# Kernel optimization log

Measured on AMD Instinct MI355X. Metric: run time of the kernel, lower is better.

Reference implementation:

```python
import jax, jax.numpy as jnp
import numpy as np

D_MODEL = 768
NUM_HEADS = 12
HEAD_DIM = D_MODEL // NUM_HEADS
B, S = 2, 2048


def setup_inputs() -> dict:
    key = jax.random.key(0)
    ks = jax.random.split(key, 12)
    s = 1.0 / np.sqrt(D_MODEL)
    inp = {
        "query": jax.random.normal(ks[0], (B, S, D_MODEL), jnp.float32),
        "key": jax.random.normal(ks[1], (B, S, D_MODEL), jnp.float32),
        "value": jax.random.normal(ks[2], (B, S, D_MODEL), jnp.float32),
        # causal mask; masked_fill(scores, mask == 0, -inf)
        "mask": jnp.tril(jnp.ones((S, S), jnp.int32))[None, None, :, :],
        "Wq": jax.random.uniform(ks[3], (D_MODEL, D_MODEL), jnp.float32, -s, s),
        "bq": jax.random.uniform(ks[4], (D_MODEL,), jnp.float32, -s, s),
        "Wk": jax.random.uniform(ks[5], (D_MODEL, D_MODEL), jnp.float32, -s, s),
        "bk": jax.random.uniform(ks[6], (D_MODEL,), jnp.float32, -s, s),
        "Wv": jax.random.uniform(ks[7], (D_MODEL, D_MODEL), jnp.float32, -s, s),
        "bv": jax.random.uniform(ks[8], (D_MODEL,), jnp.float32, -s, s),
        "Wo": jax.random.uniform(ks[9], (D_MODEL, D_MODEL), jnp.float32, -s, s),
        "bo": jax.random.uniform(ks[10], (D_MODEL,), jnp.float32, -s, s),
    }
    return inp


def reference(query, key, value, mask, Wq, bq, Wk, bk, Wv, bv, Wo, bo):
    Bq, Lq, Dm = query.shape
    Lk = key.shape[1]
    H, Dh = NUM_HEADS, HEAD_DIM
    # projections (torch Linear: x @ W.T + b), split into heads -> [B,H,L,Dh]
    q = (query @ Wq.T + bq).reshape(Bq, Lq, H, Dh).transpose(0, 2, 1, 3)
    k = (key @ Wk.T + bk).reshape(Bq, Lk, H, Dh).transpose(0, 2, 1, 3)
    v = (value @ Wv.T + bv).reshape(Bq, Lk, H, Dh).transpose(0, 2, 1, 3)
    scores = jnp.einsum("bhqd,bhkd->bhqk", q, k) / jnp.sqrt(jnp.float32(Dh))
    scores = jnp.where(mask == 0, -jnp.inf, scores)
    attn = jax.nn.softmax(scores, axis=-1)
    context = jnp.einsum("bhqk,bhkd->bhqd", attn, v)
    context = context.transpose(0, 2, 1, 3).reshape(Bq, Lq, Dm)
    return context @ Wo.T + bo
```

## Files before the change

### kernel.cpp

```cpp
#include <hip/hip_runtime.h>

#define DM    768
#define NH    12
#define NB    2
#define DHD   64
#define SQL   2048
#define MROWS 4096
#define WSZ   589824
#define XSZ   3145728
#define QSCALE 0.18033688f

typedef short  s16x8 __attribute__((ext_vector_type(8)));
typedef float  f32x4 __attribute__((ext_vector_type(4)));
typedef float  f32x16 __attribute__((ext_vector_type(16)));
typedef unsigned short u16x4 __attribute__((ext_vector_type(4)));
typedef unsigned short u16x8 __attribute__((ext_vector_type(8)));
typedef unsigned int   u32x4 __attribute__((ext_vector_type(4)));

static __device__ __forceinline__ unsigned short f2bf(float f) {
    unsigned int u = __builtin_bit_cast(unsigned int, f);
    u += 0x7FFFu + ((u >> 16) & 1u);
    return (unsigned short)(u >> 16);
}

static __device__ __forceinline__ unsigned int cvtpk1(float x, float y) {
    unsigned int r;
    asm("v_cvt_pk_bf16_f32 %0, %1, %2" : "=v"(r) : "v"(x), "v"(y));
    return r;
}

static __device__ __forceinline__ uint2 cvt2(float4 v) {
    return (uint2){cvtpk1(v.x, v.y), cvtpk1(v.z, v.w)};
}

static __device__ __forceinline__ f32x4 mfma16(s16x8 a, s16x8 b, f32x4 c) {
    return __builtin_amdgcn_mfma_f32_16x16x32_bf16(a, b, c, 0, 0, 0);
}
static __device__ __forceinline__ f32x16 mfma32(s16x8 a, s16x8 b, f32x16 c) {
    return __builtin_amdgcn_mfma_f32_32x32x16_bf16(a, b, c, 0, 0, 0);
}

__global__ __launch_bounds__(256)
void prepW(const float* __restrict__ Wq, const float* __restrict__ Wk,
           const float* __restrict__ Wv, const float* __restrict__ Wo,
           unsigned short* __restrict__ Wb)
{
    const int z = blockIdx.y;
    const float* src = (z == 0) ? Wq : (z == 1) ? Wk : (z == 2) ? Wv : Wo;
    unsigned short* d = Wb + (size_t)z * WSZ;
    const int i = blockIdx.x * 256 + threadIdx.x;
    float4 a = *reinterpret_cast<const float4*>(&src[(size_t)i * 8]);
    float4 b = *reinterpret_cast<const float4*>(&src[(size_t)i * 8 + 4]);
    uint2 p0 = cvt2(a), p1 = cvt2(b);
    u32x4 pk = {p0.x, p0.y, p1.x, p1.y};
    *reinterpret_cast<u32x4*>(&d[(size_t)i * 8]) = pk;
}

__global__ __launch_bounds__(256)
void qkv_proj(const float* __restrict__ Xq, const float* __restrict__ Xk,
              const float* __restrict__ Xv,
              const unsigned short* __restrict__ Wb,
              const float* __restrict__ bq, const float* __restrict__ bk,
              const float* __restrict__ bv,
              unsigned short* __restrict__ Qo, unsigned short* __restrict__ Ko,
              unsigned short* __restrict__ Vo)
{
    const int id  = blockIdx.x;
    const int xcd = id & 7;
    const int r0  = id >> 3;
    const int z   = r0 / 48;
    const int rem = r0 % 48;
    const int ml  = rem / 6;
    const int nb  = rem % 6;
    const int m0  = (xcd * 8 + ml) * 64;
    const int n0  = nb * 128;

    const float* X = (z == 0) ? Xq : (z == 1) ? Xk : Xv;
    const unsigned short* W = Wb + (size_t)z * WSZ;
    const float* bias = (z == 0) ? bq : (z == 1) ? bk : bv;
    unsigned short* O = (z == 0) ? Qo : (z == 1) ? Ko : Vo;

    __shared__ unsigned short As[64][72];
    __shared__ unsigned short Bs[128][72];

    const int tid  = threadIdx.x;
    const int lane = tid & 63;
    const int w    = tid >> 6;
    const int wm   = w >> 1, wn = w & 1;
    const int l15  = lane & 15, lg = lane >> 4;
    const int ar   = tid >> 2, ac = (tid & 3) << 4;
    const int br   = tid >> 1, bc = (tid & 1) << 5;

    f32x4 acc[2][4];
    #pragma unroll
    for (int i = 0; i < 2; ++i)
        #pragma unroll
        for (int j = 0; j < 4; ++j)
            acc[i][j] = (f32x4){0.f, 0.f, 0.f, 0.f};

    float4 ra[4]; u16x8 rb[4];
    #pragma unroll
    for (int i = 0; i < 4; ++i) {
        ra[i] = *reinterpret_cast<const float4*>(&X[(size_t)(m0 + ar) * DM + ac + i * 4]);
        rb[i] = *reinterpret_cast<const u16x8*>(&W[(size_t)(n0 + br) * DM + bc + i * 8]);
    }
    #pragma unroll
    for (int i = 0; i < 4; ++i) {
        *reinterpret_cast<uint2*>(&As[ar][ac + i * 4]) = cvt2(ra[i]);
        *reinterpret_cast<u16x8*>(&Bs[br][bc + i * 8]) = rb[i];
    }
    __syncthreads();

    for (int k0 = 0; k0 < DM; k0 += 64) {
        const bool more = (k0 + 64 < DM);
        if (more) {
            #pragma unroll
            for (int i = 0; i < 4; ++i) {
                ra[i] = *reinterpret_cast<const float4*>(&X[(size_t)(m0 + ar) * DM + k0 + 64 + ac + i * 4]);
                rb[i] = *reinterpret_cast<const u16x8*>(&W[(size_t)(n0 + br) * DM + k0 + 64 + bc + i * 8]);
            }
        }
        s16x8 af[2][2], bfg[4][2];
        #pragma unroll
        for (int mi = 0; mi < 2; ++mi)
            #pragma unroll
            for (int ks = 0; ks < 2; ++ks)
                af[mi][ks] = *reinterpret_cast<const s16x8*>(&As[wm * 32 + mi * 16 + l15][ks * 32 + lg * 8]);
        #pragma unroll
        for (int nj = 0; nj < 4; ++nj)
            #pragma unroll
            for (int ks = 0; ks < 2; ++ks)
                bfg[nj][ks] = *reinterpret_cast<const s16x8*>(&Bs[wn * 64 + nj * 16 + l15][ks * 32 + lg * 8]);
        #pragma unroll
        for (int mi = 0; mi < 2; ++mi)
            #pragma unroll
            for (int nj = 0; nj < 4; ++nj)
                #pragma unroll
                for (int ks = 0; ks < 2; ++ks)
                    acc[mi][nj] = mfma16(af[mi][ks], bfg[nj][ks], acc[mi][nj]);
        __syncthreads();
        if (more) {
            #pragma unroll
            for (int i = 0; i < 4; ++i) {
                *reinterpret_cast<uint2*>(&As[ar][ac + i * 4]) = cvt2(ra[i]);
                *reinterpret_cast<u16x8*>(&Bs[br][bc + i * 8]) = rb[i];
            }
            __syncthreads();
        }
    }

    const float scale = (z == 0) ? QSCALE : 1.0f;
    #pragma unroll
    for (int mi = 0; mi < 2; ++mi) {
        #pragma unroll
        for (int nj = 0; nj < 4; ++nj) {
            int col = n0 + wn * 64 + nj * 16 + l15;
            float bb = bias[col];
            int hh = col >> 6, d = col & 63;
            if (z < 2) {
                #pragma unroll
                for (int r = 0; r < 4; ++r) {
                    int row = m0 + wm * 32 + mi * 16 + (lg << 2) + r;
                    int b = row >> 11, s = row & (SQL - 1);
                    O[(((size_t)(b * NH + hh) * SQL) + s) * DHD + d] =
                        f2bf((acc[mi][nj][r] + bb) * scale);
                }
            } else {
                int row = m0 + wm * 32 + mi * 16 + (lg << 2);
                int b = row >> 11, s = row & (SQL - 1);
                u16x4 pk;
                #pragma unroll
                for (int r = 0; r < 4; ++r) pk[r] = f2bf(acc[mi][nj][r] + bb);
                *reinterpret_cast<u16x4*>(&O[(((size_t)(b * NH + hh) * DHD) + d) * SQL + s]) = pk;
            }
        }
    }
}

__global__ __launch_bounds__(512)
void attn(const unsigned short* __restrict__ Q, const unsigned short* __restrict__ K,
          const unsigned short* __restrict__ Vt, unsigned short* __restrict__ Ctx)
{
    __shared__ float Acc[8][2112];

    const int tid  = threadIdx.x;
    const int lane = tid & 63;
    const int w    = tid >> 6;
    const int hi   = lane >> 5;
    const int l31  = lane & 31;

    const int id  = blockIdx.x;
    const int xcd = id & 7;
    const int rr  = id >> 3;
    const int bh  = xcd * 3 + (rr % 3);
    const int qt  = 63 - rr / 3;
    const int q0  = qt * 32;

    const unsigned short* Qb = Q  + (size_t)bh * SQL * DHD;
    const unsigned short* Kb = K  + (size_t)bh * SQL * DHD;
    const unsigned short* Vb = Vt + (size_t)bh * DHD * SQL;

    s16x8 qf[4];
    #pragma unroll
    for (int t = 0; t < 4; ++t)
        qf[t] = *reinterpret_cast<const s16x8*>(&Qb[(size_t)(q0 + l31) * DHD + t * 16 + hi * 8]);

    f32x16 o0 = {}, o1 = {};
    float m = -__builtin_inff(), l = 0.f;
    const int nkt = (q0 >> 5) + 1;

    int cnt = (w < nkt) ? ((nkt - w + 7) >> 3) : 0;
    int kt  = w;

    s16x8 kA[4], kB[4];
    if (cnt >= 2) {
        const int ka = kt * 32, kb2 = (kt + 8) * 32;
        #pragma unroll
        for (int t = 0; t < 4; ++t) {
            kA[t] = *reinterpret_cast<const s16x8*>(&Kb[(size_t)(ka + l31) * DHD + t * 16 + hi * 8]);
            kB[t] = *reinterpret_cast<const s16x8*>(&Kb[(size_t)(kb2 + l31) * DHD + t * 16 + hi * 8]);
        }
    } else if (cnt == 1) {
        const int ka = kt * 32;
        #pragma unroll
        for (int t = 0; t < 4; ++t)
            kA[t] = *reinterpret_cast<const s16x8*>(&Kb[(size_t)(ka + l31) * DHD + t * 16 + hi * 8]);
    }

    while (cnt >= 2) {
        const int ka = kt * 32, kb2 = (kt + 8) * 32;

        s16x8 va00 = *reinterpret_cast<const s16x8*>(&Vb[(size_t)(l31)      * SQL + ka + hi * 8]);
        s16x8 va01 = *reinterpret_cast<const s16x8*>(&Vb[(size_t)(l31)      * SQL + ka + 16 + hi * 8]);
        s16x8 va10 = *reinterpret_cast<const s16x8*>(&Vb[(size_t)(32 + l31) * SQL + ka + hi * 8]);
        s16x8 va11 = *reinterpret_cast<const s16x8*>(&Vb[(size_t)(32 + l31) * SQL + ka + 16 + hi * 8]);
        s16x8 vb00 = *reinterpret_cast<const s16x8*>(&Vb[(size_t)(l31)      * SQL + kb2 + hi * 8]);
        s16x8 vb01 = *reinterpret_cast<const s16x8*>(&Vb[(size_t)(l31)      * SQL + kb2 + 16 + hi * 8]);
        s16x8 vb10 = *reinterpret_cast<const s16x8*>(&Vb[(size_t)(32 + l31) * SQL + kb2 + hi * 8]);
        s16x8 vb11 = *reinterpret_cast<const s16x8*>(&Vb[(size_t)(32 + l31) * SQL + kb2 + 16 + hi * 8]);

        f32x16 sa = {}, sb = {};
        #pragma unroll
        for (int t = 0; t < 4; ++t) sa = mfma32(kA[t], qf[t], sa);
        #pragma unroll
        for (int t = 0; t < 4; ++t) sb = mfma32(kB[t], qf[t], sb);

        const int ncnt = cnt - 2, nkt2 = kt + 16;
        if (ncnt >= 2) {
            const int na = nkt2 * 32, nb = (nkt2 + 8) * 32;
            #pragma unroll
            for (int t = 0; t < 4; ++t) {
                kA[t] = *reinterpret_cast<const s16x8*>(&Kb[(size_t)(na + l31) * DHD + t * 16 + hi * 8]);
                kB[t] = *reinterpret_cast<const s16x8*>(&Kb[(size_t)(nb + l31) * DHD + t * 16 + hi * 8]);
            }
        } else if (ncnt == 1) {
            const int na = nkt2 * 32;
            #pragma unroll
            for (int t = 0; t < 4; ++t)
                kA[t] = *reinterpret_cast<const s16x8*>(&Kb[(size_t)(na + l31) * DHD + t * 16 + hi * 8]);
        }

        if (kt + 8 == nkt - 1) {
            #pragma unroll
            for (int r = 0; r < 16; ++r) {
                int kvr = (r & 3) + 8 * (r >> 2) + 4 * hi;
                if (kvr > l31) sb[r] = -1.0e30f;
            }
        }

        float pm = fmaxf(sa[0], sb[0]);
        #pragma unroll
        for (int r = 1; r < 16; ++r) pm = fmaxf(pm, fmaxf(sa[r], sb[r]));
        pm = fmaxf(pm, __shfl_xor(pm, 32));

        if (!__all(pm <= m)) {
            const float mn = fmaxf(m, pm);
            const float al = __builtin_amdgcn_exp2f(m - mn);
            m = mn;
            l *= al;
            #pragma unroll
            for (int r = 0; r < 16; ++r) { o0[r] *= al; o1[r] *= al; }
        }

        float rs = 0.f;
        #pragma unroll
        for (int r = 0; r < 16; ++r) {
            sa[r] = __builtin_amdgcn_exp2f(sa[r] - m); rs += sa[r];
            sb[r] = __builtin_amdgcn_exp2f(sb[r] - m); rs += sb[r];
        }
        rs += __shfl_xor(rs, 32);
        l += rs;

        s16x8 pfa[2], pfb[2];
        #pragma unroll
        for (int ks = 0; ks < 2; ++ks) {
            const int rb = ks * 8;
            unsigned int a0 = cvtpk1(sa[rb + 0], sa[rb + 1]);
            unsigned int b0 = cvtpk1(sa[rb + 4], sa[rb + 5]);
            asm("v_permlane32_swap_b32 %0, %1" : "+v"(a0), "+v"(b0));
            unsigned int a1 = cvtpk1(sa[rb + 2], sa[rb + 3]);
            unsigned int b1 = cvtpk1(sa[rb + 6], sa[rb + 7]);
            asm("v_permlane32_swap_b32 %0, %1" : "+v"(a1), "+v"(b1));
            u32x4 pw = {a0, a1, b0, b1};
            pfa[ks] = __builtin_bit_cast(s16x8, pw);
        }
        #pragma unroll
        for (int ks = 0; ks < 2; ++ks) {
            const int rb = ks * 8;
            unsigned int a0 = cvtpk1(sb[rb + 0], sb[rb + 1]);
            unsigned int b0 = cvtpk1(sb[rb + 4], sb[rb + 5]);
            asm("v_permlane32_swap_b32 %0, %1" : "+v"(a0), "+v"(b0));
            unsigned int a1 = cvtpk1(sb[rb + 2], sb[rb + 3]);
            unsigned int b1 = cvtpk1(sb[rb + 6], sb[rb + 7]);
            asm("v_permlane32_swap_b32 %0, %1" : "+v"(a1), "+v"(b1));
            u32x4 pw = {a0, a1, b0, b1};
            pfb[ks] = __builtin_bit_cast(s16x8, pw);
        }

        o0 = mfma32(va00, pfa[0], o0);
        o0 = mfma32(va01, pfa[1], o0);
        o1 = mfma32(va10, pfa[0], o1);
        o1 = mfma32(va11, pfa[1], o1);
        o0 = mfma32(vb00, pfb[0], o0);
        o0 = mfma32(vb01, pfb[1], o0);
        o1 = mfma32(vb10, pfb[0], o1);
        o1 = mfma32(vb11, pfb[1], o1);

        kt = nkt2; cnt = ncnt;
    }

    if (cnt) {
        const int ka = kt * 32;
        s16x8 va00 = *reinterpret_cast<const s16x8*>(&Vb[(size_t)(l31)      * SQL + ka + hi * 8]);
        s16x8 va01 = *reinterpret_cast<const s16x8*>(&Vb[(size_t)(l31)      * SQL + ka + 16 + hi * 8]);
        s16x8 va10 = *reinterpret_cast<const s16x8*>(&Vb[(size_t)(32 + l31) * SQL + ka + hi * 8]);
        s16x8 va11 = *reinterpret_cast<const s16x8*>(&Vb[(size_t)(32 + l31) * SQL + ka + 16 + hi * 8]);

        f32x16 sa = {};
        #pragma unroll
        for (int t = 0; t < 4; ++t) sa = mfma32(kA[t], qf[t], sa);

        if (kt == nkt - 1) {
            #pragma unroll
            for (int r = 0; r < 16; ++r) {
                int kvr = (r & 3) + 8 * (r >> 2) + 4 * hi;
                if (kvr > l31) sa[r] = -1.0e30f;
            }
        }

        float pm = sa[0];
        #pragma unroll
        for (int r = 1; r < 16; ++r) pm = fmaxf(pm, sa[r]);
        pm = fmaxf(pm, __shfl_xor(pm, 32));

        if (!__all(pm <= m)) {
            const float mn = fmaxf(m, pm);
            const float al = __builtin_amdgcn_exp2f(m - mn);
            m = mn;
            l *= al;
            #pragma unroll
            for (int r = 0; r < 16; ++r) { o0[r] *= al; o1[r] *= al; }
        }

        float rs = 0.f;
        #pragma unroll
        for (int r = 0; r < 16; ++r) {
            sa[r] = __builtin_amdgcn_exp2f(sa[r] - m); rs += sa[r];
        }
        rs += __shfl_xor(rs, 32);
        l += rs;

        s16x8 pfa[2];
        #pragma unroll
        for (int ks = 0; ks < 2; ++ks) {
            const int rb = ks * 8;
            unsigned int a0 = cvtpk1(sa[rb + 0], sa[rb + 1]);
            unsigned int b0 = cvtpk1(sa[rb + 4], sa[rb + 5]);
            asm("v_permlane32_swap_b32 %0, %1" : "+v"(a0), "+v"(b0));
            unsigned int a1 = cvtpk1(sa[rb + 2], sa[rb + 3]);
            unsigned int b1 = cvtpk1(sa[rb + 6], sa[rb + 7]);
            asm("v_permlane32_swap_b32 %0, %1" : "+v"(a1), "+v"(b1));
            u32x4 pw = {a0, a1, b0, b1};
            pfa[ks] = __builtin_bit_cast(s16x8, pw);
        }

        o0 = mfma32(va00, pfa[0], o0);
        o0 = mfma32(va01, pfa[1], o0);
        o1 = mfma32(va10, pfa[0], o1);
        o1 = mfma32(va11, pfa[1], o1);
    }

    #pragma unroll
    for (int r = 0; r < 16; ++r) {
        int d = (r & 3) + 8 * (r >> 2) + 4 * hi;
        Acc[w][d * 32 + l31]        = o0[r];
        Acc[w][(32 + d) * 32 + l31] = o1[r];
    }
    if (hi == 0) { Acc[w][2048 + l31] = m; Acc[w][2080 + l31] = l; }
    __syncthreads();

    {
        const int q  = tid & 31;
        const int d4 = (tid >> 5) << 2;
        float M = -__builtin_inff();
        float mv[8];
        #pragma unroll
        for (int j = 0; j < 8; ++j) { mv[j] = Acc[j][2048 + q]; M = fmaxf(M, mv[j]); }
        float f[8]; float L = 0.f;
        #pragma unroll
        for (int j = 0; j < 8; ++j) {
            f[j] = __builtin_amdgcn_exp2f(mv[j] - M);
            L += f[j] * Acc[j][2080 + q];
        }
        const float invL = 1.0f / L;
        const int b = bh / NH, h = bh % NH;
        u16x4 pk;
        #pragma unroll
        for (int jj = 0; jj < 4; ++jj) {
            int d = d4 + jj;
            float o = 0.f;
            #pragma unroll
            for (int j = 0; j < 8; ++j) o += f[j] * Acc[j][d * 32 + q];
            pk[jj] = f2bf(o * invL);
        }
        *reinterpret_cast<u16x4*>(&Ctx[(((size_t)(b * SQL + q0 + q) * NH) + h) * DHD + d4]) = pk;
    }
}

__global__ __launch_bounds__(256)
void out_proj(const unsigned short* __restrict__ Ctx, const unsigned short* __restrict__ Wob,
              const float* __restrict__ bo, float* __restrict__ Out)
{
    __shared__ unsigned short As[64][72];
    __shared__ unsigned short Bs[64][72];

    const int id  = blockIdx.x;
    const int xcd = id & 7;
    const int r2  = id >> 3;
    const int ml  = r2 / 12;
    const int nb  = r2 % 12;
    const int m0  = (xcd * 8 + ml) * 64;
    const int n0  = nb * 64;

    const int tid  = threadIdx.x;
    const int lane = tid & 63;
    const int w    = tid >> 6;
    const int wm   = w >> 1, wn = w & 1;
    const int l15  = lane & 15, lg = lane >> 4;
    const int ar   = tid >> 2, ac = (tid & 3) << 4;

    f32x4 acc[2][2];
    #pragma unroll
    for (int i = 0; i < 2; ++i)
        #pragma unroll
        for (int j = 0; j < 2; ++j)
            acc[i][j] = (f32x4){0.f, 0.f, 0.f, 0.f};

    u16x8 ra[2], rb[2];
    #pragma unroll
    for (int i = 0; i < 2; ++i) {
        ra[i] = *reinterpret_cast<const u16x8*>(&Ctx[(size_t)(m0 + ar) * DM + ac + i * 8]);
        rb[i] = *reinterpret_cast<const u16x8*>(&Wob[(size_t)(n0 + ar) * DM + ac + i * 8]);
    }
    #pragma unroll
    for (int i = 0; i < 2; ++i) {
        *reinterpret_cast<u16x8*>(&As[ar][ac + i * 8]) = ra[i];
        *reinterpret_cast<u16x8*>(&Bs[ar][ac + i * 8]) = rb[i];
    }
    __syncthreads();

    for (int k0 = 0; k0 < DM; k0 += 64) {
        const bool more = (k0 + 64 < DM);
        if (more) {
            #pragma unroll
            for (int i = 0; i < 2; ++i) {
                ra[i] = *reinterpret_cast<const u16x8*>(&Ctx[(size_t)(m0 + ar) * DM + k0 + 64 + ac + i * 8]);
                rb[i] = *reinterpret_cast<const u16x8*>(&Wob[(size_t)(n0 + ar) * DM + k0 + 64 + ac + i * 8]);
            }
        }
        s16x8 af[2][2], bfg[2][2];
        #pragma unroll
        for (int mi = 0; mi < 2; ++mi)
            #pragma unroll
            for (int ks = 0; ks < 2; ++ks) {
                af[mi][ks]  = *reinterpret_cast<const s16x8*>(&As[wm * 32 + mi * 16 + l15][ks * 32 + lg * 8]);
                bfg[mi][ks] = *reinterpret_cast<const s16x8*>(&Bs[wn * 32 + mi * 16 + l15][ks * 32 + lg * 8]);
            }
        #pragma unroll
        for (int mi = 0; mi < 2; ++mi)
            #pragma unroll
            for (int nj = 0; nj < 2; ++nj)
                #pragma unroll
                for (int ks = 0; ks < 2; ++ks)
                    acc[mi][nj] = mfma16(af[mi][ks], bfg[nj][ks], acc[mi][nj]);
        __syncthreads();
        if (more) {
            #pragma unroll
            for (int i = 0; i < 2; ++i) {
                *reinterpret_cast<u16x8*>(&As[ar][ac + i * 8]) = ra[i];
                *reinterpret_cast<u16x8*>(&Bs[ar][ac + i * 8]) = rb[i];
            }
            __syncthreads();
        }
    }

    #pragma unroll
    for (int mi = 0; mi < 2; ++mi)
        #pragma unroll
        for (int nj = 0; nj < 2; ++nj) {
            int col = n0 + wn * 32 + nj * 16 + l15;
            float bb = bo[col];
            #pragma unroll
            for (int r = 0; r < 4; ++r) {
                int row = m0 + wm * 32 + mi * 16 + (lg << 2) + r;
                Out[(size_t)row * DM + col] = acc[mi][nj][r] + bb;
            }
        }
}

extern "C" void kernel_launch(void* const* d_in, const int* in_sizes, int n_in,
                              void* d_out, int out_size, void* d_ws, size_t ws_size,
                              hipStream_t stream) {
    const float* query = (const float*)d_in[0];
    const float* key   = (const float*)d_in[1];
    const float* value = (const float*)d_in[2];
    const float* Wq = (const float*)d_in[4];
    const float* bq = (const float*)d_in[5];
    const float* Wk = (const float*)d_in[6];
    const float* bk = (const float*)d_in[7];
    const float* Wv = (const float*)d_in[8];
    const float* bv = (const float*)d_in[9];
    const float* Wo = (const float*)d_in[10];
    const float* bo = (const float*)d_in[11];
    float* out = (float*)d_out;

    unsigned short* Wb  = (unsigned short*)d_ws;
    unsigned short* Qb  = Wb  + (size_t)4 * WSZ;
    unsigned short* Kb  = Qb  + (size_t)XSZ;
    unsigned short* Vtb = Kb  + (size_t)XSZ;
    unsigned short* Ctx = Vtb + (size_t)XSZ;

    prepW<<<dim3(288, 4), 256, 0, stream>>>(Wq, Wk, Wv, Wo, Wb);
    qkv_proj<<<dim3(1152), 256, 0, stream>>>(query, key, value, Wb,
                                             bq, bk, bv, Qb, Kb, Vtb);
    attn<<<dim3(NB * NH * 64), 512, 0, stream>>>(Qb, Kb, Vtb, Ctx);
    out_proj<<<dim3(768), 256, 0, stream>>>(Ctx, Wb + (size_t)3 * WSZ, bo, out);
}
```

Baseline: 221.9 us.

## Pre-convert activations to bf16 and use direct global-to-LDS loads in GEMMs

Activations X are now converted to bf16 in a separate prep kernel together with the weights. Both projection GEMMs then stage tiles with global_load_lds straight into unpadded 32-wide LDS tiles, using larger output tiles (128x128 for QKV, 64x128 for the output projection) and fewer blocks. The aim is to remove register staging and in-kernel conversion and to raise arithmetic intensity. The cost is an extra pass over the activations, a single-buffered K=32 loop with two barriers per step, possible LDS bank conflicts from the unpadded layout, and reuse of the Xb buffer for Ctx.

```diff
diff --git a/kernel.cpp b/kernel.cpp
--- a/kernel.cpp
+++ b/kernel.cpp
@@ -17,6 +17,9 @@
 typedef unsigned short u16x8 __attribute__((ext_vector_type(8)));
 typedef unsigned int   u32x4 __attribute__((ext_vector_type(4)));
 
+typedef const __attribute__((address_space(1))) unsigned int glb_u32;
+typedef __attribute__((address_space(3))) unsigned int lds_u32;
+
 static __device__ __forceinline__ unsigned short f2bf(float f) {
     unsigned int u = __builtin_bit_cast(unsigned int, f);
     u += 0x7FFFu + ((u >> 16) & 1u);
@@ -40,118 +43,114 @@
     return __builtin_amdgcn_mfma_f32_32x32x16_bf16(a, b, c, 0, 0, 0);
 }
 
+static __device__ __forceinline__ void gload16(const unsigned short* g, unsigned short* l) {
+    __builtin_amdgcn_global_load_lds((glb_u32*)g, (lds_u32*)l, 16, 0, 0);
+}
+
 __global__ __launch_bounds__(256)
-void prepW(const float* __restrict__ Wq, const float* __restrict__ Wk,
-           const float* __restrict__ Wv, const float* __restrict__ Wo,
-           unsigned short* __restrict__ Wb)
+void prep(const float* __restrict__ Xq, const float* __restrict__ Xk,
+          const float* __restrict__ Xv,
+          const float* __restrict__ Wq, const float* __restrict__ Wk,
+          const float* __restrict__ Wv, const float* __restrict__ Wo,
+          unsigned short* __restrict__ Xb, unsigned short* __restrict__ Wb)
 {
-    const int z = blockIdx.y;
-    const float* src = (z == 0) ? Wq : (z == 1) ? Wk : (z == 2) ? Wv : Wo;
-    unsigned short* d = Wb + (size_t)z * WSZ;
-    const int i = blockIdx.x * 256 + threadIdx.x;
-    float4 a = *reinterpret_cast<const float4*>(&src[(size_t)i * 8]);
-    float4 b = *reinterpret_cast<const float4*>(&src[(size_t)i * 8 + 4]);
-    uint2 p0 = cvt2(a), p1 = cvt2(b);
-    u32x4 pk = {p0.x, p0.y, p1.x, p1.y};
-    *reinterpret_cast<u32x4*>(&d[(size_t)i * 8]) = pk;
+    const int y = blockIdx.y;
+    const float* src;
+    unsigned short* dst;
+    int nv;
+    if (y < 3) {
+        src = (y == 0) ? Xq : (y == 1) ? Xk : Xv;
+        dst = Xb + (size_t)y * XSZ;
+        nv = XSZ / 8;
+    } else {
+        const int z = y - 3;
+        src = (z == 0) ? Wq : (z == 1) ? Wk : (z == 2) ? Wv : Wo;
+        dst = Wb + (size_t)z * WSZ;
+        nv = WSZ / 8;
+    }
+    for (int i = blockIdx.x * 256 + threadIdx.x; i < nv; i += gridDim.x * 256) {
+        float4 a = *reinterpret_cast<const float4*>(&src[(size_t)i * 8]);
+        float4 b = *reinterpret_cast<const float4*>(&src[(size_t)i * 8 + 4]);
+        uint2 p0 = cvt2(a), p1 = cvt2(b);
+        u32x4 pk = {p0.x, p0.y, p1.x, p1.y};
+        *reinterpret_cast<u32x4*>(&dst[(size_t)i * 8]) = pk;
+    }
 }
 
 __global__ __launch_bounds__(256)
-void qkv_proj(const float* __restrict__ Xq, const float* __restrict__ Xk,
-              const float* __restrict__ Xv,
+void qkv_proj(const unsigned short* __restrict__ Xb,
               const unsigned short* __restrict__ Wb,
               const float* __restrict__ bq, const float* __restrict__ bk,
               const float* __restrict__ bv,
               unsigned short* __restrict__ Qo, unsigned short* __restrict__ Ko,
               unsigned short* __restrict__ Vo)
 {
+    __shared__ unsigned short As[128][32];
+    __shared__ unsigned short Bs[128][32];
+
     const int id  = blockIdx.x;
     const int xcd = id & 7;
     const int r0  = id >> 3;
-    const int z   = r0 / 48;
-    const int rem = r0 % 48;
+    const int z   = r0 / 24;
+    const int rem = r0 % 24;
     const int ml  = rem / 6;
     const int nb  = rem % 6;
-    const int m0  = (xcd * 8 + ml) * 64;
+    const int m0  = (xcd * 4 + ml) * 128;
     const int n0  = nb * 128;
 
-    const float* X = (z == 0) ? Xq : (z == 1) ? Xk : Xv;
+    const unsigned short* X = Xb + (size_t)z * XSZ;
     const unsigned short* W = Wb + (size_t)z * WSZ;
     const float* bias = (z == 0) ? bq : (z == 1) ? bk : bv;
     unsigned short* O = (z == 0) ? Qo : (z == 1) ? Ko : Vo;
-
-    __shared__ unsigned short As[64][72];
-    __shared__ unsigned short Bs[128][72];
 
     const int tid  = threadIdx.x;
     const int lane = tid & 63;
     const int w    = tid >> 6;
     const int wm   = w >> 1, wn = w & 1;
     const int l15  = lane & 15, lg = lane >> 4;
-    const int ar   = tid >> 2, ac = (tid & 3) << 4;
-    const int br   = tid >> 1, bc = (tid & 1) << 5;
-
-    f32x4 acc[2][4];
+    const int srow = lane >> 2;
+    const int scol = (lane & 3) << 3;
+
+    f32x4 acc[4][4];
     #pragma unroll
-    for (int i = 0; i < 2; ++i)
+    for (int i = 0; i < 4; ++i)
         #pragma unroll
         for (int j = 0; j < 4; ++j)
             acc[i][j] = (f32x4){0.f, 0.f, 0.f, 0.f};
 
-    float4 ra[4]; u16x8 rb[4];
-    #pragma unroll
-    for (int i = 0; i < 4; ++i) {
-        ra[i] = *reinterpret_cast<const float4*>(&X[(size_t)(m0 + ar) * DM + ac + i * 4]);
-        rb[i] = *reinterpret_cast<const u16x8*>(&W[(size_t)(n0 + br) * DM + bc + i * 8]);
-    }
-    #pragma unroll
-    for (int i = 0; i < 4; ++i) {
-        *reinterpret_cast<uint2*>(&As[ar][ac + i * 4]) = cvt2(ra[i]);
-        *reinterpret_cast<u16x8*>(&Bs[br][bc + i * 8]) = rb[i];
-    }
-    __syncthreads();
-
-    for (int k0 = 0; k0 < DM; k0 += 64) {
-        const bool more = (k0 + 64 < DM);
-        if (more) {
-            #pragma unroll
-            for (int i = 0; i < 4; ++i) {
-                ra[i] = *reinterpret_cast<const float4*>(&X[(size_t)(m0 + ar) * DM + k0 + 64 + ac + i * 4]);
-                rb[i] = *reinterpret_cast<const u16x8*>(&W[(size_t)(n0 + br) * DM + k0 + 64 + bc + i * 8]);
-            }
-        }
-        s16x8 af[2][2], bfg[4][2];
-        #pragma unroll
-        for (int mi = 0; mi < 2; ++mi)
-            #pragma unroll
-            for (int ks = 0; ks < 2; ++ks)
-                af[mi][ks] = *reinterpret_cast<const s16x8*>(&As[wm * 32 + mi * 16 + l15][ks * 32 + lg * 8]);
+    #define QKV_STAGE(k0)                                                          \
+        {                                                                          \
+            _Pragma("unroll")                                                      \
+            for (int j = 0; j < 2; ++j) {                                          \
+                int rr = w * 32 + j * 16;                                          \
+                gload16(&X[(size_t)(m0 + rr + srow) * DM + (k0) + scol], &As[rr][0]); \
+                gload16(&W[(size_t)(n0 + rr + srow) * DM + (k0) + scol], &Bs[rr][0]); \
+            }                                                                      \
+        }
+
+    QKV_STAGE(0)
+    for (int k0 = 0; k0 < DM; k0 += 32) {
+        __syncthreads();
+        s16x8 af[4], bfg[4];
+        #pragma unroll
+        for (int mi = 0; mi < 4; ++mi)
+            af[mi] = *reinterpret_cast<const s16x8*>(&As[wm * 64 + mi * 16 + l15][lg * 8]);
         #pragma unroll
         for (int nj = 0; nj < 4; ++nj)
-            #pragma unroll
-            for (int ks = 0; ks < 2; ++ks)
-                bfg[nj][ks] = *reinterpret_cast<const s16x8*>(&Bs[wn * 64 + nj * 16 + l15][ks * 32 + lg * 8]);
-        #pragma unroll
-        for (int mi = 0; mi < 2; ++mi)
+            bfg[nj] = *reinterpret_cast<const s16x8*>(&Bs[wn * 64 + nj * 16 + l15][lg * 8]);
+        #pragma unroll
+        for (int mi = 0; mi < 4; ++mi)
             #pragma unroll
             for (int nj = 0; nj < 4; ++nj)
-                #pragma unroll
-                for (int ks = 0; ks < 2; ++ks)
-                    acc[mi][nj] = mfma16(af[mi][ks], bfg[nj][ks], acc[mi][nj]);
+                acc[mi][nj] = mfma16(af[mi], bfg[nj], acc[mi][nj]);
         __syncthreads();
-        if (more) {
-            #pragma unroll
-            for (int i = 0; i < 4; ++i) {
-                *reinterpret_cast<uint2*>(&As[ar][ac + i * 4]) = cvt2(ra[i]);
-                *reinterpret_cast<u16x8*>(&Bs[br][bc + i * 8]) = rb[i];
-            }
-            __syncthreads();
-        }
-    }
+        if (k0 + 32 < DM) QKV_STAGE(k0 + 32)
+    }
+    #undef QKV_STAGE
 
     const float scale = (z == 0) ? QSCALE : 1.0f;
     #pragma unroll
-    for (int mi = 0; mi < 2; ++mi) {
+    for (int mi = 0; mi < 4; ++mi) {
         #pragma unroll
         for (int nj = 0; nj < 4; ++nj) {
             int col = n0 + wn * 64 + nj * 16 + l15;
@@ -160,13 +159,13 @@
             if (z < 2) {
                 #pragma unroll
                 for (int r = 0; r < 4; ++r) {
-                    int row = m0 + wm * 32 + mi * 16 + (lg << 2) + r;
+                    int row = m0 + wm * 64 + mi * 16 + (lg << 2) + r;
                     int b = row >> 11, s = row & (SQL - 1);
                     O[(((size_t)(b * NH + hh) * SQL) + s) * DHD + d] =
                         f2bf((acc[mi][nj][r] + bb) * scale);
                 }
             } else {
-                int row = m0 + wm * 32 + mi * 16 + (lg << 2);
+                int row = m0 + wm * 64 + mi * 16 + (lg << 2);
                 int b = row >> 11, s = row & (SQL - 1);
                 u16x4 pk;
                 #pragma unroll
@@ -431,84 +430,68 @@
 void out_proj(const unsigned short* __restrict__ Ctx, const unsigned short* __restrict__ Wob,
               const float* __restrict__ bo, float* __restrict__ Out)
 {
-    __shared__ unsigned short As[64][72];
-    __shared__ unsigned short Bs[64][72];
+    __shared__ unsigned short As[64][32];
+    __shared__ unsigned short Bs[128][32];
 
     const int id  = blockIdx.x;
     const int xcd = id & 7;
     const int r2  = id >> 3;
-    const int ml  = r2 / 12;
-    const int nb  = r2 % 12;
+    const int ml  = r2 / 6;
+    const int nb  = r2 % 6;
     const int m0  = (xcd * 8 + ml) * 64;
-    const int n0  = nb * 64;
+    const int n0  = nb * 128;
 
     const int tid  = threadIdx.x;
     const int lane = tid & 63;
     const int w    = tid >> 6;
     const int wm   = w >> 1, wn = w & 1;
     const int l15  = lane & 15, lg = lane >> 4;
-    const int ar   = tid >> 2, ac = (tid & 3) << 4;
-
-    f32x4 acc[2][2];
+    const int srow = lane >> 2;
+    const int scol = (lane & 3) << 3;
+
+    f32x4 acc[2][4];
     #pragma unroll
     for (int i = 0; i < 2; ++i)
         #pragma unroll
-        for (int j = 0; j < 2; ++j)
+        for (int j = 0; j < 4; ++j)
             acc[i][j] = (f32x4){0.f, 0.f, 0.f, 0.f};
 
-    u16x8 ra[2], rb[2];
-    #pragma unroll
-    for (int i = 0; i < 2; ++i) {
-        ra[i] = *reinterpret_cast<const u16x8*>(&Ctx[(size_t)(m0 + ar) * DM + ac + i * 8]);
-        rb[i] = *reinterpret_cast<const u16x8*>(&Wob[(size_t)(n0 + ar) * DM + ac + i * 8]);
-    }
-    #pragma unroll
-    for (int i = 0; i < 2; ++i) {
-        *reinterpret_cast<u16x8*>(&As[ar][ac + i * 8]) = ra[i];
-        *reinterpret_cast<u16x8*>(&Bs[ar][ac + i * 8]) = rb[i];
-    }
-    __syncthreads();
-
-    for (int k0 = 0; k0 < DM; k0 += 64) {
-        const bool more = (k0 + 64 < DM);
-        if (more) {
-            #pragma unroll
-            for (int i = 0; i < 2; ++i) {
-                ra[i] = *reinterpret_cast<const u16x8*>(&Ctx[(size_t)(m0 + ar) * DM + k0 + 64 + ac + i * 8]);
-                rb[i] = *reinterpret_cast<const u16x8*>(&Wob[(size_t)(n0 + ar) * DM + k0 + 64 + ac + i * 8]);
-            }
-        }
-        s16x8 af[2][2], bfg[2][2];
+    #define OUT_STAGE(k0)                                                           \
+        {                                                                           \
+            int arr = w * 16;                                                       \
+            gload16(&Ctx[(size_t)(m0 + arr + srow) * DM + (k0) + scol], &As[arr][0]); \
+            _Pragma("unroll")                                                       \
+            for (int j = 0; j < 2; ++j) {                                           \
+                int brr = w * 32 + j * 16;                                          \
+                gload16(&Wob[(size_t)(n0 + brr + srow) * DM + (k0) + scol], &Bs[brr][0]); \
+            }                                                                       \
+        }
+
+    OUT_STAGE(0)
+    for (int k0 = 0; k0 < DM; k0 += 32) {
+        __syncthreads();
+        s16x8 af[2], bfg[4];
         #pragma unroll
         for (int mi = 0; mi < 2; ++mi)
-            #pragma unroll
-            for (int ks = 0; ks < 2; ++ks) {
-                af[mi][ks]  = *reinterpret_cast<const s16x8*>(&As[wm * 32 + mi * 16 + l15][ks * 32 + lg * 8]);
-                bfg[mi][ks] = *reinterpret_cast<const s16x8*>(&Bs[wn * 32 + mi * 16 + l15][ks * 32 + lg * 8]);
-            }
+            af[mi] = *reinterpret_cast<const s16x8*>(&As[wm * 32 + mi * 16 + l15][lg * 8]);
+        #pragma unroll
+        for (int nj = 0; nj < 4; ++nj)
+            bfg[nj] = *reinterpret_cast<const s16x8*>(&Bs[wn * 64 + nj * 16 + l15][lg * 8]);
         #pragma unroll
         for (int mi = 0; mi < 2; ++mi)
             #pragma unroll
-            for (int nj = 0; nj < 2; ++nj)
-                #pragma unroll
-                for (int ks = 0; ks < 2; ++ks)
-                    acc[mi][nj] = mfma16(af[mi][ks], bfg[nj][ks], acc[mi][nj]);
+            for (int nj = 0; nj < 4; ++nj)
+                acc[mi][nj] = mfma16(af[mi], bfg[nj], acc[mi][nj]);
         __syncthreads();
-        if (more) {
-            #pragma unroll
-            for (int i = 0; i < 2; ++i) {
-                *reinterpret_cast<u16x8*>(&As[ar][ac + i * 8]) = ra[i];
-                *reinterpret_cast<u16x8*>(&Bs[ar][ac + i * 8]) = rb[i];
-            }
-            __syncthreads();
-        }
-    }
+        if (k0 + 32 < DM) OUT_STAGE(k0 + 32)
+    }
+    #undef OUT_STAGE
 
     #pragma unroll
     for (int mi = 0; mi < 2; ++mi)
         #pragma unroll
-        for (int nj = 0; nj < 2; ++nj) {
-            int col = n0 + wn * 32 + nj * 16 + l15;
+        for (int nj = 0; nj < 4; ++nj) {
+            int col = n0 + wn * 64 + nj * 16 + l15;
             float bb = bo[col];
             #pragma unroll
             for (int r = 0; r < 4; ++r) {
@@ -535,14 +518,14 @@
     float* out = (float*)d_out;
 
     unsigned short* Wb  = (unsigned short*)d_ws;
-    unsigned short* Qb  = Wb  + (size_t)4 * WSZ;
+    unsigned short* Xb  = Wb  + (size_t)4 * WSZ;
+    unsigned short* Qb  = Xb  + (size_t)3 * XSZ;
     unsigned short* Kb  = Qb  + (size_t)XSZ;
     unsigned short* Vtb = Kb  + (size_t)XSZ;
-    unsigned short* Ctx = Vtb + (size_t)XSZ;
-
-    prepW<<<dim3(288, 4), 256, 0, stream>>>(Wq, Wk, Wv, Wo, Wb);
-    qkv_proj<<<dim3(1152), 256, 0, stream>>>(query, key, value, Wb,
-                                             bq, bk, bv, Qb, Kb, Vtb);
+    unsigned short* Ctx = Xb;
+
+    prep<<<dim3(384, 7), 256, 0, stream>>>(query, key, value, Wq, Wk, Wv, Wo, Xb, Wb);
+    qkv_proj<<<dim3(576), 256, 0, stream>>>(Xb, Wb, bq, bk, bv, Qb, Kb, Vtb);
     attn<<<dim3(NB * NH * 64), 512, 0, stream>>>(Qb, Kb, Vtb, Ctx);
-    out_proj<<<dim3(768), 256, 0, stream>>>(Ctx, Wb + (size_t)3 * WSZ, bo, out);
-}
+    out_proj<<<dim3(384), 256, 0, stream>>>(Ctx, Wb + (size_t)3 * WSZ, bo, out);
+}
```

New measurement: 212.2 us. -4.4%, faster.
